# Performance work log

Hardware: AMD Instinct MI355X
Metric: run time of the kernel (lower is better)

The kernel has to match this reference:

```python
import jax, jax.numpy as jnp
import numpy as np

B, C, W, H, Z = 2, 32, 96, 96, 64
IC = C  # inter_channels defaults to in_channels (required by depthwise g conv)
THRESH = 1.5
EPS = 1e-5


def setup_inputs() -> dict:
    key = jax.random.key(0)
    ks = jax.random.split(key, 12)
    s1 = 1.0 / np.sqrt(C)   # 1x1x1 conv fan-in
    s3 = 1.0 / np.sqrt(3.0) # depthwise (1,1,3) conv fan-in per channel
    return {
        "x": jax.random.normal(ks[0], (B, C, W, H, Z), jnp.float32),
        # per-sample spacings in [0,3): mixes both branches around thresh 1.5
        "spacings": jax.random.uniform(ks[1], (B, 3), jnp.float32) * 3.0,
        "theta_w": jax.random.normal(ks[2], (IC, C), jnp.float32) * s1,
        "theta_b": jax.random.normal(ks[3], (IC,), jnp.float32) * s1,
        "phi_w": jax.random.normal(ks[4], (IC, C), jnp.float32) * s1,
        "phi_b": jax.random.normal(ks[5], (IC,), jnp.float32) * s1,
        "g_w": jax.random.normal(ks[6], (C, 3), jnp.float32) * s3,   # depthwise kernel along z
        "g_b": jax.random.normal(ks[7], (C,), jnp.float32) * s3,
        "W_w": jax.random.normal(ks[8], (C, IC), jnp.float32) * s1,
        "W_b": jax.random.normal(ks[9], (C,), jnp.float32) * s1,
        # torch inits BN gamma=0, beta=0 (zero-init residual trick); use small random
        "bn_gamma": jax.random.normal(ks[10], (C,), jnp.float32) * 0.1,
        "bn_beta": jax.random.normal(ks[11], (C,), jnp.float32) * 0.1,
    }


def _cvec(v):
    return v.reshape(1, -1, 1, 1, 1)


def _conv1x1(h, w, b):
    # 1x1x1 Conv3d == channel-mixing matmul
    return jnp.einsum('bcwhz,oc->bowhz', h, w) + _cvec(b)


def reference(x, spacings, theta_w, theta_b, phi_w, phi_b, g_w, g_b, W_w, W_b, bn_gamma, bn_beta):
    # theta/phi: 1x1x1 convs -> (B, IC, W, H, Z)
    t = _conv1x1(x, theta_w, theta_b)
    p = _conv1x1(x, phi_w, phi_b)

    # g: depthwise conv along z, kernel 3, pad 1 (groups=C)
    xp = jnp.pad(x, ((0, 0), (0, 0), (0, 0), (0, 0), (1, 1)))
    gx = (xp[..., :-2] * _cvec(g_w[:, 0])
          + xp[..., 1:-1] * _cvec(g_w[:, 1])
          + xp[..., 2:] * _cvec(g_w[:, 2])
          + _cvec(g_b))

    # non-local attention along z per (b, w, h) row: scores (B, W, H, Z, Z)
    f = jnp.einsum('bcwhz,bcwhy->bwhzy', t, p)
    a = jax.nn.softmax(f, axis=-1)
    y = jnp.einsum('bwhzy,bcwhy->bcwhz', a, gx)
    nl = y + x  # residual inside compute_x

    # per-sample branch on z-spacing, vectorized with where
    mask = (spacings[:, -1] <= THRESH).reshape(-1, 1, 1, 1, 1)
    res = jnp.where(mask, nl, x)

    # W: 1x1x1 conv + BatchNorm3d (training-mode batch stats)
    out = _conv1x1(res, W_w, W_b)
    mean = jnp.mean(out, axis=(0, 2, 3, 4), keepdims=True)
    var = jnp.var(out, axis=(0, 2, 3, 4), keepdims=True)
    out = (out - mean) * jax.lax.rsqrt(var + EPS)
    return out * _cvec(bn_gamma) + _cvec(bn_beta)
```

## Files before the change

kernel.cpp:

```cpp
#include <hip/hip_runtime.h>
#include <stdint.h>

#define CHS 589824
#define ROWS 18432
#define WHn 9216
#define NRED 1179648.0f

typedef short s16x8 __attribute__((ext_vector_type(8)));
typedef float f32x4v __attribute__((ext_vector_type(4)));

#define MFMA16 __builtin_amdgcn_mfma_f32_16x16x32_bf16

#define WSFRAG 10240

#define OX  0
#define OT  8320
#define OTL 12928
#define OP  17536
#define OG  22144
#define LDSZ 26752
#define OA  OT
#define ORT OP
#define OO  OT

static __device__ __forceinline__ uint16_t bfh(float v) {
    union { __bf16 h; uint16_t u; } c; c.h = (__bf16)v; return c.u;
}
static __device__ __forceinline__ float bf2f(uint16_t u) {
    union { uint32_t x; float f; } c; c.x = (uint32_t)u << 16; return c.f;
}
static __device__ __forceinline__ uint32_t pk2u(uint16_t a, uint16_t b) {
    return (uint32_t)a | ((uint32_t)b << 16);
}
static __device__ __forceinline__ uint32_t pkbf(float a, float b) {
    return pk2u(bfh(a), bfh(b));
}

static __device__ __forceinline__ void wfrag2(const float* __restrict__ Wp, int mt, int l15, int kb,
                                              s16x8& hi, s16x8& lo) {
    const float* p = Wp + (l15 + 16*mt)*32 + 8*kb;
    const float4 f0 = *(const float4*)p;
    const float4 f1 = *(const float4*)(p + 4);
    float f[8] = {f0.x, f0.y, f0.z, f0.w, f1.x, f1.y, f1.z, f1.w};
    union { uint32_t u[4]; s16x8 v; } rh, rl;
    #pragma unroll
    for (int i = 0; i < 4; ++i) {
        const uint16_t h0 = bfh(f[2*i]), h1 = bfh(f[2*i+1]);
        rh.u[i] = pk2u(h0, h1);
        rl.u[i] = pk2u(bfh(f[2*i] - bf2f(h0)), bfh(f[2*i+1] - bf2f(h1)));
    }
    hi = rh.v; lo = rl.v;
}
static __device__ __forceinline__ s16x8 wfragh(const float* __restrict__ Wp, int mt, int l15, int kb) {
    const float* p = Wp + (l15 + 16*mt)*32 + 8*kb;
    const float4 f0 = *(const float4*)p;
    const float4 f1 = *(const float4*)(p + 4);
    union { uint32_t u[4]; s16x8 v; } r;
    r.u[0] = pkbf(f0.x, f0.y); r.u[1] = pkbf(f0.z, f0.w);
    r.u[2] = pkbf(f1.x, f1.y); r.u[3] = pkbf(f1.z, f1.w);
    return r.v;
}

__global__ __launch_bounds__(256) void k0_frag(
    const float* __restrict__ theta_w, const float* __restrict__ phi_w,
    const float* __restrict__ Ww, char* __restrict__ ws)
{
    const int tid = threadIdx.x;
    const int m = tid >> 7;
    const int r = tid & 127;
    const int mt = r >> 6, l = r & 63;
    s16x8 hi, lo;
    wfrag2(m ? phi_w : theta_w, mt, l & 15, l >> 4, hi, lo);
    *(s16x8*)(ws + m*4096 + (mt*64 + l)*16)        = hi;
    *(s16x8*)(ws + m*4096 + 2048 + (mt*64 + l)*16) = lo;
    if (tid < 128) {
        const int mtw = tid >> 6, lw = tid & 63;
        *(s16x8*)(ws + 8192 + (mtw*64 + lw)*16) = wfragh(Ww, mtw, lw & 15, lw >> 4);
    }
}

static __device__ __forceinline__ void xfrag(const char* lds, int z, int kb, s16x8& hi, s16x8& lo) {
    union { uint32_t u[4]; s16x8 s; } H, L;
    #pragma unroll
    for (int i = 0; i < 4; ++i) {
        const float v0 = *(const float*)(lds + OX + (8*kb + 2*i    )*260 + z*4);
        const float v1 = *(const float*)(lds + OX + (8*kb + 2*i + 1)*260 + z*4);
        const uint16_t h0 = bfh(v0), h1 = bfh(v1);
        H.u[i] = pk2u(h0, h1);
        L.u[i] = pk2u(bfh(v0 - bf2f(h0)), bfh(v1 - bf2f(h1)));
    }
    hi = H.s; lo = L.s;
}
static __device__ __forceinline__ s16x8 rd72(const char* p) {
    union { uint64_t q[2]; s16x8 s; } v;
    v.q[0] = *(const uint64_t*)p;
    v.q[1] = *(const uint64_t*)(p + 8);
    return v.s;
}

__global__ __launch_bounds__(256, 6) void k1_row(
    const float* __restrict__ x, const float* __restrict__ spacings,
    const float* __restrict__ theta_b, const float* __restrict__ phi_b,
    const float* __restrict__ g_w, const float* __restrict__ g_b,
    const float* __restrict__ Wb, const char* __restrict__ frags,
    float* __restrict__ out, float* __restrict__ part)
{
    __shared__ __align__(16) char lds[LDSZ];
    const int t = threadIdx.x;
    const int wv = t >> 6, l = t & 63;
    const int l15 = l & 15, kb = l >> 4;
    const int row = blockIdx.x;
    const int b = row / WHn, wh = row - b*WHn;
    const long base = (long)b*32*CHS + (long)wh*64;
    const int zr = 16*wv + l15;

    #pragma unroll
    for (int j = 0; j < 8; ++j) {
        const int c = 8*wv + j;
        *(float*)(lds + OX + c*260 + l*4) = x[base + (long)c*CHS + l];
    }
    __syncthreads();

    #pragma unroll
    for (int j = 0; j < 8; ++j) {
        const int c = 8*wv + j;
        const float xc = *(const float*)(lds + OX + c*260 + l*4);
        const int lm = (l > 0) ? l-1 : 0, lp = (l < 63) ? l+1 : 63;
        float xm = *(const float*)(lds + OX + c*260 + lm*4);
        float xp = *(const float*)(lds + OX + c*260 + lp*4);
        if (l == 0)  xm = 0.f;
        if (l == 63) xp = 0.f;
        const float g = g_w[3*c]*xm + g_w[3*c+1]*xc + g_w[3*c+2]*xp + g_b[c];
        *(uint16_t*)(lds + OG + c*144 + 2*l) = bfh(g);
    }
    {
        const char* fb = frags + ((wv < 2) ? 0 : 4096);
        const float* wbp = (wv < 2) ? theta_b : phi_b;
        const int    dst = (wv < 2) ? OT : OP;
        const bool   doLo = (wv < 2);
        const int    ntb = (wv & 1) * 2;
        const s16x8 a0h = *(const s16x8*)(fb + l*16);
        const s16x8 a0l = *(const s16x8*)(fb + 2048 + l*16);
        const s16x8 a1h = *(const s16x8*)(fb + 1024 + l*16);
        const s16x8 a1l = *(const s16x8*)(fb + 2048 + 1024 + l*16);
        const float4 b0 = *(const float4*)(wbp + 4*kb);
        const float4 b1 = *(const float4*)(wbp + 16 + 4*kb);
        #pragma unroll
        for (int n2 = 0; n2 < 2; ++n2) {
            const int z = 16*(ntb + n2) + l15;
            s16x8 bxh, bxl;
            xfrag(lds, z, kb, bxh, bxl);
            f32x4v a0; a0[0]=b0.x; a0[1]=b0.y; a0[2]=b0.z; a0[3]=b0.w;
            f32x4v a1; a1[0]=b1.x; a1[1]=b1.y; a1[2]=b1.z; a1[3]=b1.w;
            a0 = MFMA16(a0h, bxh, a0, 0, 0, 0);
            a0 = MFMA16(a0h, bxl, a0, 0, 0, 0);
            a0 = MFMA16(a0l, bxh, a0, 0, 0, 0);
            a1 = MFMA16(a1h, bxh, a1, 0, 0, 0);
            a1 = MFMA16(a1h, bxl, a1, 0, 0, 0);
            a1 = MFMA16(a1l, bxh, a1, 0, 0, 0);
            uint16_t h[8];
            #pragma unroll
            for (int r = 0; r < 4; ++r) { h[r] = bfh(a0[r]); h[4+r] = bfh(a1[r]); }
            union { uint32_t u[2]; uint64_t q; } w0, w1;
            w0.u[0] = pk2u(h[0], h[1]); w0.u[1] = pk2u(h[2], h[3]);
            w1.u[0] = pk2u(h[4], h[5]); w1.u[1] = pk2u(h[6], h[7]);
            *(uint64_t*)(lds + dst + z*72 + 8*kb)      = w0.q;
            *(uint64_t*)(lds + dst + z*72 + 32 + 8*kb) = w1.q;
            if (doLo) {
                #pragma unroll
                for (int r = 0; r < 4; ++r) {
                    w0.u[0] = r ? w0.u[0] : 0;
                }
                union { uint32_t u[2]; uint64_t q; } v0, v1;
                v0.u[0] = pkbf(a0[0]-bf2f(h[0]), a0[1]-bf2f(h[1]));
                v0.u[1] = pkbf(a0[2]-bf2f(h[2]), a0[3]-bf2f(h[3]));
                v1.u[0] = pkbf(a1[0]-bf2f(h[4]), a1[1]-bf2f(h[5]));
                v1.u[1] = pkbf(a1[2]-bf2f(h[6]), a1[3]-bf2f(h[7]));
                *(uint64_t*)(lds + OTL + z*72 + 8*kb)      = v0.q;
                *(uint64_t*)(lds + OTL + z*72 + 32 + 8*kb) = v1.q;
            }
        }
    }
    __syncthreads();

    f32x4v Fq[4];
    {
        const s16x8 bth = rd72(lds + OT  + zr*72 + kb*16);
        const s16x8 btl = rd72(lds + OTL + zr*72 + kb*16);
        #pragma unroll
        for (int yt = 0; yt < 4; ++yt) {
            const int y = 16*yt + l15;
            const s16x8 pah = rd72(lds + OP + y*72 + kb*16);
            f32x4v zz; zz[0]=0.f; zz[1]=0.f; zz[2]=0.f; zz[3]=0.f;
            zz = MFMA16(pah, bth, zz, 0, 0, 0);
            zz = MFMA16(pah, btl, zz, 0, 0, 0);
            Fq[yt] = zz;
        }
    }
    __syncthreads();

    {
        float mx = -3.4e38f;
        #pragma unroll
        for (int yt = 0; yt < 4; ++yt)
            #pragma unroll
            for (int r = 0; r < 4; ++r) mx = fmaxf(mx, Fq[yt][r]);
        mx = fmaxf(mx, __shfl_xor(mx, 16));
        mx = fmaxf(mx, __shfl_xor(mx, 32));
        float p[4][4]; float sum = 0.f;
        #pragma unroll
        for (int yt = 0; yt < 4; ++yt)
            #pragma unroll
            for (int r = 0; r < 4; ++r) { p[yt][r] = __expf(Fq[yt][r] - mx); sum += p[yt][r]; }
        sum += __shfl_xor(sum, 16);
        sum += __shfl_xor(sum, 32);
        const float inv = 1.0f / sum;
        #pragma unroll
        for (int yt = 0; yt < 4; ++yt) {
            *(uint32_t*)(lds + OA + zr*144 + (16*yt + 4*kb)*2)     = pkbf(p[yt][0]*inv, p[yt][1]*inv);
            *(uint32_t*)(lds + OA + zr*144 + (16*yt + 4*kb)*2 + 4) = pkbf(p[yt][2]*inv, p[yt][3]*inv);
        }
    }

    {
        f32x4v Yq[2];
        #pragma unroll
        for (int r = 0; r < 4; ++r) { Yq[0][r] = 0.f; Yq[1][r] = 0.f; }
        #pragma unroll
        for (int ks = 0; ks < 2; ++ks) {
            const s16x8 bA = *(const s16x8*)(lds + OA + zr*144 + 64*ks + 16*kb);
            #pragma unroll
            for (int mt = 0; mt < 2; ++mt) {
                const s16x8 gA = *(const s16x8*)(lds + OG + (16*mt + l15)*144 + 64*ks + 16*kb);
                Yq[mt] = MFMA16(gA, bA, Yq[mt], 0, 0, 0);
            }
        }
        const bool msk = spacings[b*3 + 2] <= 1.5f;
        #pragma unroll
        for (int mt = 0; mt < 2; ++mt) {
            float rv[4];
            #pragma unroll
            for (int r = 0; r < 4; ++r) {
                const int c = 16*mt + 4*kb + r;
                const float xv = *(const float*)(lds + OX + c*260 + zr*4);
                rv[r] = msk ? (Yq[mt][r] + xv) : xv;
            }
            union { uint32_t u[2]; uint64_t q; } w;
            w.u[0] = pkbf(rv[0], rv[1]); w.u[1] = pkbf(rv[2], rv[3]);
            *(uint64_t*)(lds + ORT + zr*72 + 32*mt + 8*kb) = w.q;
        }
    }
    __syncthreads();

    {
        const s16x8 bR = rd72(lds + ORT + zr*72 + kb*16);
        #pragma unroll
        for (int mt = 0; mt < 2; ++mt) {
            const s16x8 aW = *(const s16x8*)(frags + 8192 + (mt*64 + l)*16);
            const float4 wb4 = *(const float4*)(Wb + 16*mt + 4*kb);
            f32x4v acc; acc[0]=wb4.x; acc[1]=wb4.y; acc[2]=wb4.z; acc[3]=wb4.w;
            acc = MFMA16(aW, bR, acc, 0, 0, 0);
            #pragma unroll
            for (int r = 0; r < 4; ++r)
                *(float*)(lds + OO + zr*132 + (16*mt + 4*kb + r)*4) = acc[r];
        }
    }
    __syncthreads();

    #pragma unroll
    for (int k = 0; k < 8; ++k) {
        const int o = wv + 4*k;
        const float v = *(const float*)(lds + OO + l*132 + o*4);
        out[base + (long)o*CHS + l] = v;
        float s1 = v, s2 = v*v;
        #pragma unroll
        for (int off = 32; off >= 1; off >>= 1) {
            s1 += __shfl_xor(s1, off);
            s2 += __shfl_xor(s2, off);
        }
        if (l == 0) {
            part[row*64 + o]      = s1;
            part[row*64 + 32 + o] = s2;
        }
    }
}

__global__ __launch_bounds__(256) void k2a(const float* __restrict__ part,
                                           float* __restrict__ part2)
{
    __shared__ float red[4][64];
    const int t = threadIdx.x, lane = t & 63, grp = t >> 6;
    const int p = blockIdx.x;
    float s = 0.f;
    for (int k = 0; k < 18; ++k) s += part[(p*72 + grp + 4*k)*64 + lane];
    red[grp][lane] = s;
    __syncthreads();
    if (t < 64) part2[p*64 + t] = red[0][t] + red[1][t] + red[2][t] + red[3][t];
}

__global__ __launch_bounds__(256) void k2b(const float* __restrict__ part2,
    const float* __restrict__ gamma, const float* __restrict__ beta,
    float* __restrict__ sc)
{
    __shared__ float red[4][64];
    __shared__ float tot[64];
    const int t = threadIdx.x, lane = t & 63, grp = t >> 6;
    float s = 0.f;
    for (int k = 0; k < 64; ++k) s += part2[(grp + 4*k)*64 + lane];
    red[grp][lane] = s;
    __syncthreads();
    if (t < 64) tot[t] = red[0][t] + red[1][t] + red[2][t] + red[3][t];
    __syncthreads();
    if (t < 32) {
        const float mean = tot[t] / NRED;
        const float var  = tot[32+t] / NRED - mean*mean;
        const float rstd = rsqrtf(var + 1e-5f);
        const float scale = gamma[t] * rstd;
        sc[t]    = scale;
        sc[32+t] = fmaf(-mean, scale, beta[t]);
    }
}

__global__ __launch_bounds__(256) void k3_norm(float* __restrict__ out,
                                               const float* __restrict__ sc)
{
    __shared__ float s[64];
    if (threadIdx.x < 64) s[threadIdx.x] = sc[threadIdx.x];
    __syncthreads();
    const int total4 = 2*32*CHS/4;
    const int Q = CHS/4;
    for (int i = blockIdx.x*256 + threadIdx.x; i < total4; i += gridDim.x*256) {
        float4 v = ((const float4*)out)[i];
        const int c = (i / Q) & 31;
        const float scale = s[c], shift = s[32+c];
        v.x = fmaf(v.x, scale, shift);
        v.y = fmaf(v.y, scale, shift);
        v.z = fmaf(v.z, scale, shift);
        v.w = fmaf(v.w, scale, shift);
        ((float4*)out)[i] = v;
    }
}

extern "C" void kernel_launch(void* const* d_in, const int* in_sizes, int n_in,
                              void* d_out, int out_size, void* d_ws, size_t ws_size,
                              hipStream_t stream) {
    const float* x        = (const float*)d_in[0];
    const float* spacings = (const float*)d_in[1];
    const float* theta_w  = (const float*)d_in[2];
    const float* theta_b  = (const float*)d_in[3];
    const float* phi_w    = (const float*)d_in[4];
    const float* phi_b    = (const float*)d_in[5];
    const float* g_w      = (const float*)d_in[6];
    const float* g_b      = (const float*)d_in[7];
    const float* Ww       = (const float*)d_in[8];
    const float* Wb       = (const float*)d_in[9];
    const float* gamma    = (const float*)d_in[10];
    const float* beta     = (const float*)d_in[11];
    float* out   = (float*)d_out;
    char*  frags = (char*)d_ws;
    float* part  = (float*)((char*)d_ws + WSFRAG);
    float* part2 = part + ROWS*64;
    float* sc    = part2 + 256*64;

    hipLaunchKernelGGL(k0_frag, dim3(1), dim3(256), 0, stream, theta_w, phi_w, Ww, frags);
    hipLaunchKernelGGL(k1_row, dim3(ROWS), dim3(256), 0, stream,
                       x, spacings, theta_b, phi_b, g_w, g_b, Wb, frags, out, part);
    hipLaunchKernelGGL(k2a, dim3(256), dim3(256), 0, stream, part, part2);
    hipLaunchKernelGGL(k2b, dim3(1), dim3(256), 0, stream, part2, gamma, beta, sc);
    hipLaunchKernelGGL(k3_norm, dim3(4096), dim3(256), 0, stream, out, sc);
}
```

Before: 196.2 us.

## Store x tile as pre-split bf16 hi/lo and use shuffles for depthwise conv

Each thread converts its loaded x values to bf16 hi/lo pairs once and writes them in a z-major LDS layout. MFMA B fragments are then read with plain vector loads instead of eight scalar loads plus conversions. The depthwise z-conv gets its neighbours via __shfl_up/down from registers, which removes one barrier and the fp32 LDS staging. The residual now uses the bf16-rounded x value, which slightly changes numerics before the W conv.

After: 201.4 us. +2.7%, slower.

```diff
diff --git a/kernel.cpp b/kernel.cpp
--- a/kernel.cpp
+++ b/kernel.cpp
@@ -13,12 +13,12 @@
 
 #define WSFRAG 10240
 
-#define OX  0
-#define OT  8320
-#define OTL 12928
-#define OP  17536
-#define OG  22144
-#define LDSZ 26752
+#define OXH 0
+#define OT  8704
+#define OTL 13312
+#define OP  17920
+#define OG  22528
+#define LDSZ 27136
 #define OA  OT
 #define ORT OP
 #define OO  OT
@@ -34,6 +34,12 @@
 }
 static __device__ __forceinline__ uint32_t pkbf(float a, float b) {
     return pk2u(bfh(a), bfh(b));
+}
+static __device__ __forceinline__ s16x8 rd8(const char* p) {
+    union { uint64_t q[2]; s16x8 s; } v;
+    v.q[0] = *(const uint64_t*)p;
+    v.q[1] = *(const uint64_t*)(p + 8);
+    return v.s;
 }
 
 static __device__ __forceinline__ void wfrag2(const float* __restrict__ Wp, int mt, int l15, int kb,
@@ -79,25 +85,6 @@
     }
 }
 
-static __device__ __forceinline__ void xfrag(const char* lds, int z, int kb, s16x8& hi, s16x8& lo) {
-    union { uint32_t u[4]; s16x8 s; } H, L;
-    #pragma unroll
-    for (int i = 0; i < 4; ++i) {
-        const float v0 = *(const float*)(lds + OX + (8*kb + 2*i    )*260 + z*4);
-        const float v1 = *(const float*)(lds + OX + (8*kb + 2*i + 1)*260 + z*4);
-        const uint16_t h0 = bfh(v0), h1 = bfh(v1);
-        H.u[i] = pk2u(h0, h1);
-        L.u[i] = pk2u(bfh(v0 - bf2f(h0)), bfh(v1 - bf2f(h1)));
-    }
-    hi = H.s; lo = L.s;
-}
-static __device__ __forceinline__ s16x8 rd72(const char* p) {
-    union { uint64_t q[2]; s16x8 s; } v;
-    v.q[0] = *(const uint64_t*)p;
-    v.q[1] = *(const uint64_t*)(p + 8);
-    return v.s;
-}
-
 __global__ __launch_bounds__(256, 6) void k1_row(
     const float* __restrict__ x, const float* __restrict__ spacings,
     const float* __restrict__ theta_b, const float* __restrict__ phi_b,
@@ -114,25 +101,26 @@
     const long base = (long)b*32*CHS + (long)wh*64;
     const int zr = 16*wv + l15;
 
+    float xv[8];
+    #pragma unroll
+    for (int j = 0; j < 8; ++j) xv[j] = x[base + (long)(8*wv + j)*CHS + l];
+    #pragma unroll
+    for (int j = 0; j < 4; ++j) {
+        const uint16_t h0 = bfh(xv[2*j]), h1 = bfh(xv[2*j+1]);
+        *(uint32_t*)(lds + OXH + l*136 + (8*wv + 2*j)*2)      = pk2u(h0, h1);
+        *(uint32_t*)(lds + OXH + l*136 + 64 + (8*wv + 2*j)*2) =
+            pk2u(bfh(xv[2*j] - bf2f(h0)), bfh(xv[2*j+1] - bf2f(h1)));
+    }
     #pragma unroll
     for (int j = 0; j < 8; ++j) {
         const int c = 8*wv + j;
-        *(float*)(lds + OX + c*260 + l*4) = x[base + (long)c*CHS + l];
-    }
-    __syncthreads();
-
-    #pragma unroll
-    for (int j = 0; j < 8; ++j) {
-        const int c = 8*wv + j;
-        const float xc = *(const float*)(lds + OX + c*260 + l*4);
-        const int lm = (l > 0) ? l-1 : 0, lp = (l < 63) ? l+1 : 63;
-        float xm = *(const float*)(lds + OX + c*260 + lm*4);
-        float xp = *(const float*)(lds + OX + c*260 + lp*4);
-        if (l == 0)  xm = 0.f;
-        if (l == 63) xp = 0.f;
-        const float g = g_w[3*c]*xm + g_w[3*c+1]*xc + g_w[3*c+2]*xp + g_b[c];
+        float xm = __shfl_up(xv[j], 1);   if (l == 0)  xm = 0.f;
+        float xp = __shfl_down(xv[j], 1); if (l == 63) xp = 0.f;
+        const float g = g_w[3*c]*xm + g_w[3*c+1]*xv[j] + g_w[3*c+2]*xp + g_b[c];
         *(uint16_t*)(lds + OG + c*144 + 2*l) = bfh(g);
     }
+    __syncthreads();
+
     {
         const char* fb = frags + ((wv < 2) ? 0 : 4096);
         const float* wbp = (wv < 2) ? theta_b : phi_b;
@@ -140,16 +128,16 @@
         const bool   doLo = (wv < 2);
         const int    ntb = (wv & 1) * 2;
         const s16x8 a0h = *(const s16x8*)(fb + l*16);
+        const s16x8 a1h = *(const s16x8*)(fb + 1024 + l*16);
         const s16x8 a0l = *(const s16x8*)(fb + 2048 + l*16);
-        const s16x8 a1h = *(const s16x8*)(fb + 1024 + l*16);
-        const s16x8 a1l = *(const s16x8*)(fb + 2048 + 1024 + l*16);
+        const s16x8 a1l = *(const s16x8*)(fb + 3072 + l*16);
         const float4 b0 = *(const float4*)(wbp + 4*kb);
         const float4 b1 = *(const float4*)(wbp + 16 + 4*kb);
         #pragma unroll
         for (int n2 = 0; n2 < 2; ++n2) {
             const int z = 16*(ntb + n2) + l15;
-            s16x8 bxh, bxl;
-            xfrag(lds, z, kb, bxh, bxl);
+            const s16x8 bxh = rd8(lds + OXH + z*136 + 16*kb);
+            const s16x8 bxl = rd8(lds + OXH + z*136 + 64 + 16*kb);
             f32x4v a0; a0[0]=b0.x; a0[1]=b0.y; a0[2]=b0.z; a0[3]=b0.w;
             f32x4v a1; a1[0]=b1.x; a1[1]=b1.y; a1[2]=b1.z; a1[3]=b1.w;
             a0 = MFMA16(a0h, bxh, a0, 0, 0, 0);
@@ -167,10 +155,6 @@
             *(uint64_t*)(lds + dst + z*72 + 8*kb)      = w0.q;
             *(uint64_t*)(lds + dst + z*72 + 32 + 8*kb) = w1.q;
             if (doLo) {
-                #pragma unroll
-                for (int r = 0; r < 4; ++r) {
-                    w0.u[0] = r ? w0.u[0] : 0;
-                }
                 union { uint32_t u[2]; uint64_t q; } v0, v1;
                 v0.u[0] = pkbf(a0[0]-bf2f(h[0]), a0[1]-bf2f(h[1]));
                 v0.u[1] = pkbf(a0[2]-bf2f(h[2]), a0[3]-bf2f(h[3]));
@@ -185,12 +169,12 @@
 
     f32x4v Fq[4];
     {
-        const s16x8 bth = rd72(lds + OT  + zr*72 + kb*16);
-        const s16x8 btl = rd72(lds + OTL + zr*72 + kb*16);
+        const s16x8 bth = rd8(lds + OT  + zr*72 + 16*kb);
+        const s16x8 btl = rd8(lds + OTL + zr*72 + 16*kb);
         #pragma unroll
         for (int yt = 0; yt < 4; ++yt) {
             const int y = 16*yt + l15;
-            const s16x8 pah = rd72(lds + OP + y*72 + kb*16);
+            const s16x8 pah = rd8(lds + OP + y*72 + 16*kb);
             f32x4v zz; zz[0]=0.f; zz[1]=0.f; zz[2]=0.f; zz[3]=0.f;
             zz = MFMA16(pah, bth, zz, 0, 0, 0);
             zz = MFMA16(pah, btl, zz, 0, 0, 0);
@@ -238,12 +222,12 @@
         const bool msk = spacings[b*3 + 2] <= 1.5f;
         #pragma unroll
         for (int mt = 0; mt < 2; ++mt) {
+            const uint64_t xh = *(const uint64_t*)(lds + OXH + zr*136 + (16*mt + 4*kb)*2);
             float rv[4];
             #pragma unroll
             for (int r = 0; r < 4; ++r) {
-                const int c = 16*mt + 4*kb + r;
-                const float xv = *(const float*)(lds + OX + c*260 + zr*4);
-                rv[r] = msk ? (Yq[mt][r] + xv) : xv;
+                const float xr = bf2f((uint16_t)(xh >> (16*r)));
+                rv[r] = msk ? (Yq[mt][r] + xr) : xr;
             }
             union { uint32_t u[2]; uint64_t q; } w;
             w.u[0] = pkbf(rv[0], rv[1]); w.u[1] = pkbf(rv[2], rv[3]);
@@ -253,7 +237,7 @@
     __syncthreads();
 
     {
-        const s16x8 bR = rd72(lds + ORT + zr*72 + kb*16);
+        const s16x8 bR = rd8(lds + ORT + zr*72 + 16*kb);
         #pragma unroll
         for (int mt = 0; mt < 2; ++mt) {
             const s16x8 aW = *(const s16x8*)(frags + 8192 + (mt*64 + l)*16);
```
